# Optimization experiments

Measured on AMD Instinct MI355X. Metric: run time of the kernel, lower is better.

Reference implementation:

```python
import jax, jax.numpy as jnp
import numpy as np

N_NODES = 50000
N_EDGES = 1600000
N_GRAPHS = 128
DIM_IN = 128
DIM_SELF = 16


def setup_inputs() -> dict:
    key = jax.random.key(0)
    ks = jax.random.split(key, 12)
    feat = jax.random.normal(ks[0], (N_NODES, DIM_IN), dtype=jnp.float32)
    self_feat = jax.random.normal(ks[1], (N_GRAPHS, DIM_SELF), dtype=jnp.float32)
    src = jax.random.randint(ks[2], (N_EDGES,), 0, N_NODES)
    dst = jax.random.randint(ks[3], (N_EDGES,), 0, N_NODES)
    graph_id = jnp.sort(jax.random.randint(ks[4], (N_NODES,), 0, N_GRAPHS))
    def lin(k, fan_in, fan_out):
        bound = 1.0 / np.sqrt(fan_in)
        return jax.random.uniform(k, (fan_in, fan_out), dtype=jnp.float32, minval=-bound, maxval=bound)
    W1 = lin(ks[5], DIM_IN, 100)
    b1 = jnp.zeros((100,), jnp.float32)
    W2 = lin(ks[6], 100, 20)
    b2 = jnp.zeros((20,), jnp.float32)
    Wf1 = lin(ks[7], 20 + DIM_SELF, 10)
    bf1 = jnp.zeros((10,), jnp.float32)
    Wf2 = lin(ks[8], 10, 1)
    bf2 = jnp.zeros((1,), jnp.float32)
    return {"feat": feat, "self_feat": self_feat, "src": src, "dst": dst,
            "graph_id": graph_id, "W1": W1, "b1": b1, "W2": W2, "b2": b2,
            "Wf1": Wf1, "bf1": bf1, "Wf2": Wf2, "bf2": bf2}


def _gcn_layer(h, src, dst, deg, W, b):
    # copy_u gather over edges + mean segment reduce over dst, then linear apply
    msg_sum = jax.ops.segment_sum(h[src], dst, num_segments=h.shape[0])  # [N, d]
    mean = msg_sum / jnp.maximum(deg, 1.0)[:, None]
    # DGL update_all leaves zero-in-degree nodes with their prior feature
    h_agg = jnp.where((deg > 0)[:, None], mean, h)
    return h_agg @ W + b


def reference(feat, self_feat, src, dst, graph_id, W1, b1, W2, b2, Wf1, bf1, Wf2, bf2):
    n = feat.shape[0]
    deg = jax.ops.segment_sum(jnp.ones((src.shape[0],), feat.dtype), dst, num_segments=n)
    h = jax.nn.relu(_gcn_layer(feat, src, dst, deg, W1, b1))   # [N,100]
    h = jax.nn.relu(_gcn_layer(h, src, dst, deg, W2, b2))      # [N,20]
    # dgl.mean_nodes: per-graph mean of node features
    g_sum = jax.ops.segment_sum(h, graph_id, num_segments=N_GRAPHS)  # [G,20]
    g_cnt = jax.ops.segment_sum(jnp.ones((n,), h.dtype), graph_id, num_segments=N_GRAPHS)
    hg = g_sum / jnp.maximum(g_cnt, 1.0)[:, None]
    fused = jnp.concatenate([hg, self_feat], axis=1)           # [G, 20+dim_self]
    out = jax.nn.relu(fused @ Wf1 + bf1) @ Wf2 + bf2           # [G, dim_out]
    return out
```

## Files before the change

### kernel.cpp

```cpp
#include <hip/hip_runtime.h>

constexpr int NN = 50000;
constexpr int NE = 1600000;
constexpr int NG = 128;
constexpr int BSTRIDE = 96;

constexpr int FILL_PASSES = 8;
constexpr int NODES_PER_PASS = 6250;
constexpr int FILL_CHUNKS = 6250;
constexpr int G1_PERIOD = 41;
constexpr int G1_SLOT = 20;
constexpr int G1_VBLOCKS = 1250;
constexpr int TOTAL_SUPERS = 6417;
constexpr int FUSED_BLOCKS = TOTAL_SUPERS * 8;

constexpr int A1_NODES = 16;
constexpr int A1_BLOCKS = NN / A1_NODES;
constexpr int A2_BLOCKS = NN / 16;

#define OFF_CNT      0
#define OFF_GSUM     200000
#define OFF_GCNT     210240
#define ZERO_BYTES   210752
#define OFF_ADJ      210752
#define OFF_X1F      9810816
#define OFF_X2B      16210816

typedef float v2f __attribute__((ext_vector_type(2)));

__device__ __forceinline__ unsigned short f2bf(float x) {
    unsigned int v = __float_as_uint(x);
    return (unsigned short)((v + 0x7FFFu + ((v >> 16) & 1u)) >> 16);
}
__device__ __forceinline__ float bflo(unsigned int u) { return __uint_as_float(u << 16); }
__device__ __forceinline__ float bfhi(unsigned int u) { return __uint_as_float(u & 0xFFFF0000u); }

__global__ __launch_bounds__(256) void k_fill_gemm1(
        const int* __restrict__ src, const int* __restrict__ dst,
        int* __restrict__ cnt, unsigned short* __restrict__ adj,
        const float4* __restrict__ feat4, const float* __restrict__ W1,
        unsigned int* __restrict__ X1f) {
    const unsigned int super = blockIdx.x >> 3;
    const unsigned int lane8 = blockIdx.x & 7;
    const unsigned int qq = super / G1_PERIOD;
    const unsigned int rr = super - qq * G1_PERIOD;

    if (rr != G1_SLOT) {
        const int chunk = (int)(super - qq - (rr > G1_SLOT ? 1u : 0u));
        if (chunk >= FILL_CHUNKS) return;
        const int i = chunk * 256 + threadIdx.x;
        const int d = dst[i];
        const int lo = (int)lane8 * NODES_PER_PASS;
        if (d >= lo && d < lo + NODES_PER_PASS) {
            const int p = atomicAdd(&cnt[d], 1);
            if (p < BSTRIDE) adj[d * BSTRIDE + p] = (unsigned short)src[i];
        }
        return;
    }

    const int gb = (int)(qq * 8 + lane8);
    if (gb >= G1_VBLOCKS) return;
    const int t = threadIdx.x;
    if (t >= 250) return;
    const int cg = t % 25;
    const int nq = t / 25;
    const int node0 = gb * 40 + nq * 4;
    const int col0 = cg * 4;

    float acc[4][4];
#pragma unroll
    for (int i = 0; i < 4; ++i)
#pragma unroll
        for (int j = 0; j < 4; ++j) acc[i][j] = 0.f;

    for (int k4 = 0; k4 < 32; ++k4) {
        float4 f[4];
#pragma unroll
        for (int i = 0; i < 4; ++i) f[i] = feat4[(node0 + i) * 32 + k4];
        float4 wr[4];
#pragma unroll
        for (int kk = 0; kk < 4; ++kk)
            wr[kk] = *(const float4*)(W1 + (k4 * 4 + kk) * 100 + col0);
#pragma unroll
        for (int kk = 0; kk < 4; ++kk) {
#pragma unroll
            for (int i = 0; i < 4; ++i) {
                const float fv = (kk == 0) ? f[i].x
                               : (kk == 1) ? f[i].y
                               : (kk == 2) ? f[i].z : f[i].w;
                acc[i][0] += fv * wr[kk].x;
                acc[i][1] += fv * wr[kk].y;
                acc[i][2] += fv * wr[kk].z;
                acc[i][3] += fv * wr[kk].w;
            }
        }
    }
#pragma unroll
    for (int i = 0; i < 4; ++i) {
        int u = 0;
        u = __builtin_amdgcn_cvt_pk_fp8_f32(acc[i][0], acc[i][1], u, false);
        u = __builtin_amdgcn_cvt_pk_fp8_f32(acc[i][2], acc[i][3], u, true);
        X1f[(node0 + i) * 32 + cg] = (unsigned int)u;
        if (cg == 24) {
#pragma unroll
            for (int z = 25; z < 32; ++z) X1f[(node0 + i) * 32 + z] = 0u;
        }
    }
}

__global__ __launch_bounds__(256) void k_agg1g2(
        const uint4* __restrict__ X1u, const int* __restrict__ cnt,
        const unsigned short* __restrict__ adj, const float* __restrict__ b1,
        const float* __restrict__ W2, unsigned int* __restrict__ X2b) {
    __shared__ float hl[A1_NODES * 100];
    __shared__ float w2s[100 * 20];
    const int t = threadIdx.x;
    const int node0 = blockIdx.x * A1_NODES;
    for (int i = t; i < 2000; i += 256) w2s[i] = W2[i];

    const int nl   = t >> 4;
    const int l    = t & 15;
    const int q    = l & 7;
    const int half = l >> 3;
    const int node = node0 + nl;
    const int d = cnt[node];
    const unsigned short* ab = adj + node * BSTRIDE;
    float a[16];
#pragma unroll
    for (int j = 0; j < 16; ++j) a[j] = 0.f;

#define ACC4(UU, B) { v2f l_ = __builtin_amdgcn_cvt_pk_f32_fp8((int)(UU), false); \
                      v2f h_ = __builtin_amdgcn_cvt_pk_f32_fp8((int)(UU), true);  \
                      a[B+0] += l_.x; a[B+1] += l_.y; a[B+2] += h_.x; a[B+3] += h_.y; }
#define SET4(UU, B) { v2f l_ = __builtin_amdgcn_cvt_pk_f32_fp8((int)(UU), false); \
                      v2f h_ = __builtin_amdgcn_cvt_pk_f32_fp8((int)(UU), true);  \
                      a[B+0] = l_.x; a[B+1] = l_.y; a[B+2] = h_.x; a[B+3] = h_.y; }
#define ACCU4(U) ACC4((U).x, 0) ACC4((U).y, 4) ACC4((U).z, 8) ACC4((U).w, 12)

    if (q < 7) {
        if (d == 0) {
            if (half == 0) {
                const uint4 u = X1u[node * 8 + q];
                SET4(u.x, 0) SET4(u.y, 4) SET4(u.z, 8) SET4(u.w, 12)
            }
        } else {
            const int m  = (d >> 1) & ~3;
            const int i0 = half ? m : 0;
            const int i1 = half ? d : m;
            int i = i0;
            for (; i + 4 <= i1; i += 4) {
                const ushort4 s4 = *(const ushort4*)(ab + i);
                const uint4 u0 = X1u[(int)s4.x * 8 + q];
                const uint4 u1 = X1u[(int)s4.y * 8 + q];
                const uint4 u2 = X1u[(int)s4.z * 8 + q];
                const uint4 u3 = X1u[(int)s4.w * 8 + q];
                ACCU4(u0) ACCU4(u1) ACCU4(u2) ACCU4(u3)
            }
            for (; i < i1; ++i) {
                const uint4 u = X1u[(int)ab[i] * 8 + q];
                ACCU4(u)
            }
        }
    }
#undef ACCU4
#undef ACC4
#undef SET4
#pragma unroll
    for (int j = 0; j < 16; ++j) a[j] += __shfl_xor(a[j], 8);

    if (half == 0 && q < 7) {
        if (d > 0) {
            const float inv = 1.f / (float)d;
#pragma unroll
            for (int j = 0; j < 16; ++j) a[j] *= inv;
        }
        const int col0 = 16 * q;
        float* hrow = hl + nl * 100 + col0;
        const int nc = (q < 6) ? 16 : 4;
#pragma unroll 4
        for (int j = 0; j < nc; ++j)
            hrow[j] = fmaxf(a[j] + b1[col0 + j], 0.f);
    }
    __syncthreads();

    const int j = t & 15;
    unsigned int o = 0u;
    if (j < 10) {
        const float* h = hl + nl * 100;
        float a0 = 0.f, a1 = 0.f;
#pragma unroll 5
        for (int k = 0; k < 100; ++k) {
            const float hv = h[k];
            a0 += hv * w2s[k * 20 + 2 * j];
            a1 += hv * w2s[k * 20 + 2 * j + 1];
        }
        o = (unsigned int)f2bf(a0) | ((unsigned int)f2bf(a1) << 16);
    }
    X2b[node * 16 + j] = o;
}

__global__ __launch_bounds__(256) void k_agg2(const uint2* __restrict__ X2v,
                                              const int* __restrict__ cnt,
                                              const unsigned short* __restrict__ adj,
                                              const float* __restrict__ b2,
                                              const int* __restrict__ graph_id,
                                              float* __restrict__ g_sum,
                                              float* __restrict__ g_cnt) {
    __shared__ float lsum[NG * 20];
    __shared__ float lcnt[NG];
    const int t = threadIdx.x;
    for (int i = t; i < NG * 20; i += 256) lsum[i] = 0.f;
    if (t < NG) lcnt[t] = 0.f;
    __syncthreads();

    const int nl   = t >> 4;
    const int l    = t & 15;
    const int q    = l & 7;
    const int half = l >> 3;
    const int node = blockIdx.x * 16 + nl;
    const int d = cnt[node];
    const unsigned short* ab = adj + node * BSTRIDE;
    float ax = 0.f, ay = 0.f, az = 0.f, aw = 0.f;
#define ACCU2(U) { ax += bflo((U).x); ay += bfhi((U).x); \
                   az += bflo((U).y); aw += bfhi((U).y); }
    if (q < 5) {
        if (d == 0) {
            if (half == 0) {
                const uint2 u = X2v[node * 8 + q];
                ax = bflo(u.x); ay = bfhi(u.x);
                az = bflo(u.y); aw = bfhi(u.y);
            }
        } else {
            const int m  = (d >> 1) & ~3;
            const int i0 = half ? m : 0;
            const int i1 = half ? d : m;
            int i = i0;
            for (; i + 4 <= i1; i += 4) {
                const ushort4 s4 = *(const ushort4*)(ab + i);
                const uint2 u0 = X2v[(int)s4.x * 8 + q];
                const uint2 u1 = X2v[(int)s4.y * 8 + q];
                const uint2 u2 = X2v[(int)s4.z * 8 + q];
                const uint2 u3 = X2v[(int)s4.w * 8 + q];
                ACCU2(u0) ACCU2(u1) ACCU2(u2) ACCU2(u3)
            }
            for (; i < i1; ++i) {
                const uint2 u = X2v[(int)ab[i] * 8 + q];
                ACCU2(u)
            }
        }
    }
#undef ACCU2
    ax += __shfl_xor(ax, 8);
    ay += __shfl_xor(ay, 8);
    az += __shfl_xor(az, 8);
    aw += __shfl_xor(aw, 8);

    if (half == 0 && q < 5) {
        if (d > 0) {
            const float inv = 1.f / (float)d;
            ax *= inv; ay *= inv; az *= inv; aw *= inv;
        }
        const int col0 = 4 * q;
        const float hx = fmaxf(ax + b2[col0 + 0], 0.f);
        const float hy = fmaxf(ay + b2[col0 + 1], 0.f);
        const float hz = fmaxf(az + b2[col0 + 2], 0.f);
        const float hw = fmaxf(aw + b2[col0 + 3], 0.f);
        const int g = graph_id[node];
        atomicAdd(&lsum[g * 20 + col0 + 0], hx);
        atomicAdd(&lsum[g * 20 + col0 + 1], hy);
        atomicAdd(&lsum[g * 20 + col0 + 2], hz);
        atomicAdd(&lsum[g * 20 + col0 + 3], hw);
    }
    if (l == 0) atomicAdd(&lcnt[graph_id[node]], 1.f);
    __syncthreads();

    const int first = blockIdx.x * 16;
    const int gmin = graph_id[first];
    const int span = graph_id[first + 15] - gmin + 1;
    for (int idx = t; idx < span * 20; idx += 256) {
        const int g = gmin + idx / 20;
        const int c = idx - (idx / 20) * 20;
        const float v = lsum[g * 20 + c];
        if (v != 0.f) atomicAdd(&g_sum[g * 20 + c], v);
    }
    for (int idx = t; idx < span; idx += 256) {
        const float v = lcnt[gmin + idx];
        if (v != 0.f) atomicAdd(&g_cnt[gmin + idx], v);
    }
}

__global__ __launch_bounds__(128) void k_final(const float* __restrict__ g_sum,
                                               const float* __restrict__ g_cnt,
                                               const float* __restrict__ self_feat,
                                               const float* __restrict__ Wf1,
                                               const float* __restrict__ bf1,
                                               const float* __restrict__ Wf2,
                                               const float* __restrict__ bf2,
                                               float* __restrict__ out) {
    const int g = threadIdx.x;
    float fused[36];
    const float cnt = fmaxf(g_cnt[g], 1.f);
    const float inv = 1.f / cnt;
#pragma unroll
    for (int j = 0; j < 20; ++j) fused[j] = g_sum[g * 20 + j] * inv;
#pragma unroll
    for (int j = 0; j < 16; ++j) fused[20 + j] = self_feat[g * 16 + j];
    float o = bf2[0];
#pragma unroll
    for (int i = 0; i < 10; ++i) {
        float t = bf1[i];
#pragma unroll
        for (int k = 0; k < 36; ++k) t += fused[k] * Wf1[k * 10 + i];
        o += fmaxf(t, 0.f) * Wf2[i];
    }
    out[g] = o;
}

extern "C" void kernel_launch(void* const* d_in, const int* in_sizes, int n_in,
                              void* d_out, int out_size, void* d_ws, size_t ws_size,
                              hipStream_t stream) {
    const float* feat      = (const float*)d_in[0];
    const float* self_feat = (const float*)d_in[1];
    const int*   src       = (const int*)d_in[2];
    const int*   dst       = (const int*)d_in[3];
    const int*   graph_id  = (const int*)d_in[4];
    const float* W1        = (const float*)d_in[5];
    const float* b1        = (const float*)d_in[6];
    const float* W2        = (const float*)d_in[7];
    const float* b2        = (const float*)d_in[8];
    const float* Wf1       = (const float*)d_in[9];
    const float* bf1       = (const float*)d_in[10];
    const float* Wf2       = (const float*)d_in[11];
    const float* bf2       = (const float*)d_in[12];

    char* w = (char*)d_ws;
    int*            cnt      = (int*)(w + OFF_CNT);
    float*          g_sum    = (float*)(w + OFF_GSUM);
    float*          g_cnt    = (float*)(w + OFF_GCNT);
    unsigned short* adj      = (unsigned short*)(w + OFF_ADJ);
    unsigned int*   X1f      = (unsigned int*)(w + OFF_X1F);
    unsigned int*   X2b      = (unsigned int*)(w + OFF_X2B);

    hipMemsetAsync(w, 0, ZERO_BYTES, stream);

    k_fill_gemm1<<<FUSED_BLOCKS, 256, 0, stream>>>(src, dst, cnt, adj,
                                                   (const float4*)feat, W1, X1f);
    k_agg1g2<<<A1_BLOCKS, 256, 0, stream>>>((const uint4*)X1f, cnt, adj, b1,
                                            W2, X2b);
    k_agg2<<<A2_BLOCKS, 256, 0, stream>>>((const uint2*)X2b, cnt,
                                          adj, b2, graph_id, g_sum, g_cnt);
    k_final<<<1, 128, 0, stream>>>(g_sum, g_cnt, self_feat, Wf1, bf1, Wf2, bf2,
                                   (float*)d_out);
}
```

Before: 260.6 us.

## Split fill from GEMM1, use bf16 MFMA for GEMM1, unroll gathers by 8

Breaks the interleaved fill/GEMM1 kernel into a standalone CSR fill kernel and a separate GEMM1 kernel. The new GEMM1 converts features and W1 to bf16 on the fly and runs them through 16x16x32 MFMA instructions. The aggregation loops in both GCN layers now gather 8 neighbours per iteration for more memory-level parallelism. Splitting the kernels gives up the overlap of the atomic-bound fill with GEMM1, adds a launch, and uses bf16 inputs where GEMM1 was fp32 before.

After: 263.4 us. About the same (+1.1%).

```diff
diff --git a/kernel.cpp b/kernel.cpp
--- a/kernel.cpp
+++ b/kernel.cpp
@@ -7,12 +7,9 @@
 
 constexpr int FILL_PASSES = 8;
 constexpr int NODES_PER_PASS = 6250;
-constexpr int FILL_CHUNKS = 6250;
-constexpr int G1_PERIOD = 41;
-constexpr int G1_SLOT = 20;
-constexpr int G1_VBLOCKS = 1250;
-constexpr int TOTAL_SUPERS = 6417;
-constexpr int FUSED_BLOCKS = TOTAL_SUPERS * 8;
+constexpr int BLOCKS_PER_PASS = (NE + 255) / 256;
+
+constexpr int G1M_BLOCKS = (NN + 63) / 64;
 
 constexpr int A1_NODES = 16;
 constexpr int A1_BLOCKS = NN / A1_NODES;
@@ -27,6 +24,8 @@
 #define OFF_X2B      16210816
 
 typedef float v2f __attribute__((ext_vector_type(2)));
+typedef short bf16x8 __attribute__((ext_vector_type(8)));
+typedef float f32x4 __attribute__((ext_vector_type(4)));
 
 __device__ __forceinline__ unsigned short f2bf(float x) {
     unsigned int v = __float_as_uint(x);
@@ -35,77 +34,69 @@
 __device__ __forceinline__ float bflo(unsigned int u) { return __uint_as_float(u << 16); }
 __device__ __forceinline__ float bfhi(unsigned int u) { return __uint_as_float(u & 0xFFFF0000u); }
 
-__global__ __launch_bounds__(256) void k_fill_gemm1(
-        const int* __restrict__ src, const int* __restrict__ dst,
-        int* __restrict__ cnt, unsigned short* __restrict__ adj,
-        const float4* __restrict__ feat4, const float* __restrict__ W1,
-        unsigned int* __restrict__ X1f) {
-    const unsigned int super = blockIdx.x >> 3;
-    const unsigned int lane8 = blockIdx.x & 7;
-    const unsigned int qq = super / G1_PERIOD;
-    const unsigned int rr = super - qq * G1_PERIOD;
-
-    if (rr != G1_SLOT) {
-        const int chunk = (int)(super - qq - (rr > G1_SLOT ? 1u : 0u));
-        if (chunk >= FILL_CHUNKS) return;
-        const int i = chunk * 256 + threadIdx.x;
-        const int d = dst[i];
-        const int lo = (int)lane8 * NODES_PER_PASS;
-        if (d >= lo && d < lo + NODES_PER_PASS) {
-            const int p = atomicAdd(&cnt[d], 1);
-            if (p < BSTRIDE) adj[d * BSTRIDE + p] = (unsigned short)src[i];
-        }
-        return;
-    }
-
-    const int gb = (int)(qq * 8 + lane8);
-    if (gb >= G1_VBLOCKS) return;
+__global__ void k_fill(const int* __restrict__ src, const int* __restrict__ dst,
+                       int* __restrict__ cnt, unsigned short* __restrict__ adj) {
+    const int pass = blockIdx.x & 7;
+    const int chunk = blockIdx.x >> 3;
+    const int i = chunk * 256 + threadIdx.x;
+    if (i >= NE) return;
+    const int d = dst[i];
+    const int lo = pass * NODES_PER_PASS;
+    if (d >= lo && d < lo + NODES_PER_PASS) {
+        const int p = atomicAdd(&cnt[d], 1);
+        if (p < BSTRIDE) adj[d * BSTRIDE + p] = (unsigned short)src[i];
+    }
+}
+
+__global__ __launch_bounds__(256) void k_gemm1m(const float* __restrict__ feat,
+                                                const float* __restrict__ W1,
+                                                unsigned int* __restrict__ X1f) {
     const int t = threadIdx.x;
-    if (t >= 250) return;
-    const int cg = t % 25;
-    const int nq = t / 25;
-    const int node0 = gb * 40 + nq * 4;
-    const int col0 = cg * 4;
-
-    float acc[4][4];
-#pragma unroll
-    for (int i = 0; i < 4; ++i)
-#pragma unroll
-        for (int j = 0; j < 4; ++j) acc[i][j] = 0.f;
-
-    for (int k4 = 0; k4 < 32; ++k4) {
-        float4 f[4];
-#pragma unroll
-        for (int i = 0; i < 4; ++i) f[i] = feat4[(node0 + i) * 32 + k4];
-        float4 wr[4];
-#pragma unroll
-        for (int kk = 0; kk < 4; ++kk)
-            wr[kk] = *(const float4*)(W1 + (k4 * 4 + kk) * 100 + col0);
-#pragma unroll
-        for (int kk = 0; kk < 4; ++kk) {
-#pragma unroll
-            for (int i = 0; i < 4; ++i) {
-                const float fv = (kk == 0) ? f[i].x
-                               : (kk == 1) ? f[i].y
-                               : (kk == 2) ? f[i].z : f[i].w;
-                acc[i][0] += fv * wr[kk].x;
-                acc[i][1] += fv * wr[kk].y;
-                acc[i][2] += fv * wr[kk].z;
-                acc[i][3] += fv * wr[kk].w;
-            }
-        }
-    }
-#pragma unroll
-    for (int i = 0; i < 4; ++i) {
-        int u = 0;
-        u = __builtin_amdgcn_cvt_pk_fp8_f32(acc[i][0], acc[i][1], u, false);
-        u = __builtin_amdgcn_cvt_pk_fp8_f32(acc[i][2], acc[i][3], u, true);
-        X1f[(node0 + i) * 32 + cg] = (unsigned int)u;
-        if (cg == 24) {
-#pragma unroll
-            for (int z = 25; z < 32; ++z) X1f[(node0 + i) * 32 + z] = 0u;
-        }
-    }
+    const int wv = t >> 6;
+    const int l  = t & 63;
+    const int ln16 = l & 15;
+    const int lh   = l >> 4;
+    const int node = blockIdx.x * 64 + wv * 16 + ln16;
+    const bool live = (node < NN);
+
+    bf16x8 bfr[4];
+#pragma unroll
+    for (int ks = 0; ks < 4; ++ks) {
+        float4 f0 = {0.f,0.f,0.f,0.f}, f1 = {0.f,0.f,0.f,0.f};
+        if (live) {
+            f0 = *(const float4*)(feat + node * 128 + ks * 32 + lh * 8);
+            f1 = *(const float4*)(feat + node * 128 + ks * 32 + lh * 8 + 4);
+        }
+        bf16x8 b;
+        b[0] = (short)f2bf(f0.x); b[1] = (short)f2bf(f0.y);
+        b[2] = (short)f2bf(f0.z); b[3] = (short)f2bf(f0.w);
+        b[4] = (short)f2bf(f1.x); b[5] = (short)f2bf(f1.y);
+        b[6] = (short)f2bf(f1.z); b[7] = (short)f2bf(f1.w);
+        bfr[ks] = b;
+    }
+
+#pragma unroll
+    for (int ct = 0; ct < 7; ++ct) {
+        const int col = ct * 16 + ln16;
+        f32x4 acc = {0.f, 0.f, 0.f, 0.f};
+#pragma unroll
+        for (int ks = 0; ks < 4; ++ks) {
+            bf16x8 a;
+#pragma unroll
+            for (int j = 0; j < 8; ++j) {
+                const int k = ks * 32 + lh * 8 + j;
+                a[j] = (col < 100) ? (short)f2bf(W1[k * 100 + col]) : (short)0;
+            }
+            acc = __builtin_amdgcn_mfma_f32_16x16x32_bf16(a, bfr[ks], acc, 0, 0, 0);
+        }
+        if (live) {
+            int u = 0;
+            u = __builtin_amdgcn_cvt_pk_fp8_f32(acc[0], acc[1], u, false);
+            u = __builtin_amdgcn_cvt_pk_fp8_f32(acc[2], acc[3], u, true);
+            X1f[node * 32 + ct * 4 + lh] = (unsigned int)u;
+        }
+    }
+    if (live) X1f[node * 32 + 28 + lh] = 0u;
 }
 
 __global__ __launch_bounds__(256) void k_agg1g2(
@@ -148,6 +139,20 @@
             const int i0 = half ? m : 0;
             const int i1 = half ? d : m;
             int i = i0;
+            for (; i + 8 <= i1; i += 8) {
+                const ushort4 sa = *(const ushort4*)(ab + i);
+                const ushort4 sb = *(const ushort4*)(ab + i + 4);
+                const uint4 u0 = X1u[(int)sa.x * 8 + q];
+                const uint4 u1 = X1u[(int)sa.y * 8 + q];
+                const uint4 u2 = X1u[(int)sa.z * 8 + q];
+                const uint4 u3 = X1u[(int)sa.w * 8 + q];
+                const uint4 u4 = X1u[(int)sb.x * 8 + q];
+                const uint4 u5 = X1u[(int)sb.y * 8 + q];
+                const uint4 u6 = X1u[(int)sb.z * 8 + q];
+                const uint4 u7 = X1u[(int)sb.w * 8 + q];
+                ACCU4(u0) ACCU4(u1) ACCU4(u2) ACCU4(u3)
+                ACCU4(u4) ACCU4(u5) ACCU4(u6) ACCU4(u7)
+            }
             for (; i + 4 <= i1; i += 4) {
                 const ushort4 s4 = *(const ushort4*)(ab + i);
                 const uint4 u0 = X1u[(int)s4.x * 8 + q];
@@ -183,10 +188,11 @@
     }
     __syncthreads();
 
+    const int nl2 = t >> 4;
     const int j = t & 15;
     unsigned int o = 0u;
     if (j < 10) {
-        const float* h = hl + nl * 100;
+        const float* h = hl + nl2 * 100;
         float a0 = 0.f, a1 = 0.f;
 #pragma unroll 5
         for (int k = 0; k < 100; ++k) {
@@ -196,7 +202,7 @@
         }
         o = (unsigned int)f2bf(a0) | ((unsigned int)f2bf(a1) << 16);
     }
-    X2b[node * 16 + j] = o;
+    X2b[(node0 + nl2) * 16 + j] = o;
 }
 
 __global__ __launch_bounds__(256) void k_agg2(const uint2* __restrict__ X2v,
@@ -235,6 +241,20 @@
             const int i0 = half ? m : 0;
             const int i1 = half ? d : m;
             int i = i0;
+            for (; i + 8 <= i1; i += 8) {
+                const ushort4 sa = *(const ushort4*)(ab + i);
+                const ushort4 sb = *(const ushort4*)(ab + i + 4);
+                const uint2 u0 = X2v[(int)sa.x * 8 + q];
+                const uint2 u1 = X2v[(int)sa.y * 8 + q];
+                const uint2 u2 = X2v[(int)sa.z * 8 + q];
+                const uint2 u3 = X2v[(int)sa.w * 8 + q];
+                const uint2 u4 = X2v[(int)sb.x * 8 + q];
+                const uint2 u5 = X2v[(int)sb.y * 8 + q];
+                const uint2 u6 = X2v[(int)sb.z * 8 + q];
+                const uint2 u7 = X2v[(int)sb.w * 8 + q];
+                ACCU2(u0) ACCU2(u1) ACCU2(u2) ACCU2(u3)
+                ACCU2(u4) ACCU2(u5) ACCU2(u6) ACCU2(u7)
+            }
             for (; i + 4 <= i1; i += 4) {
                 const ushort4 s4 = *(const ushort4*)(ab + i);
                 const uint2 u0 = X2v[(int)s4.x * 8 + q];
@@ -343,8 +363,8 @@
 
     hipMemsetAsync(w, 0, ZERO_BYTES, stream);
 
-    k_fill_gemm1<<<FUSED_BLOCKS, 256, 0, stream>>>(src, dst, cnt, adj,
-                                                   (const float4*)feat, W1, X1f);
+    k_fill<<<FILL_PASSES * BLOCKS_PER_PASS, 256, 0, stream>>>(src, dst, cnt, adj);
+    k_gemm1m<<<G1M_BLOCKS, 256, 0, stream>>>(feat, W1, X1f);
     k_agg1g2<<<A1_BLOCKS, 256, 0, stream>>>((const uint4*)X1f, cnt, adj, b1,
                                             W2, X2b);
     k_agg2<<<A2_BLOCKS, 256, 0, stream>>>((const uint2*)X2b, cnt,
```
